# Performance work log

Hardware: AMD Instinct MI355X
Metric: run time of the kernel (lower is better)

## Reference

```python
import jax, jax.numpy as jnp
import numpy as np

H = 8            # num_heads
SIM_THRESH = 0.75


def setup_inputs() -> dict:
    key = jax.random.key(0)
    ks = jax.random.split(key, 6)
    B, N, C, CR = 1, 1536, 256, 64
    x_cls = jax.random.normal(ks[0], (B, N, C), dtype=jnp.float32)
    x_reg = jax.random.normal(ks[1], (B, N, CR), dtype=jnp.float32)
    cls_score = jax.random.uniform(ks[2], (N,), dtype=jnp.float32)
    fg_score = jax.random.uniform(ks[3], (1, 1, 1, N), dtype=jnp.float32)
    W_cls = jax.random.normal(ks[4], (C, 3 * C), dtype=jnp.float32) / np.sqrt(C).astype(np.float32)
    W_reg = jax.random.normal(ks[5], (CR, 3 * CR), dtype=jnp.float32) / np.sqrt(CR).astype(np.float32)
    return {"x_cls": x_cls, "x_reg": x_reg, "cls_score": cls_score,
            "fg_score": fg_score, "W_cls": W_cls, "W_reg": W_reg}


def _l2norm(t):
    return t / jnp.linalg.norm(t, axis=-1, keepdims=True)


def _split_qkv(x, W):
    B, N, C = x.shape
    qkv = (x @ W).reshape(B, N, 3, H, C // H).transpose(2, 0, 3, 1, 4)  # [3,B,H,N,hd]
    return qkv[0], qkv[1], qkv[2]


def reference(x_cls, x_reg, cls_score, fg_score, W_cls, W_reg):
    B, N, C = x_cls.shape
    CR = x_reg.shape[-1]
    scale = (C // H) ** -0.5  # note: torch code uses the cls head_dim scale for BOTH branches

    q, k, v = _split_qkv(x_cls, W_cls)
    qn, kn, vn = _l2norm(q), _l2norm(k), _l2norm(v)
    qr, kr, vr = _split_qkv(x_reg, W_reg)
    qrn, krn, vrn = _l2norm(qr), _l2norm(kr), _l2norm(vr)

    # cls_score broadcast: value cls_score[j] at position (i, j), as in torch's reshape+repeat
    cs = cls_score.reshape(1, 1, 1, N)
    cls_mask = (cs > jnp.swapaxes(cs, -2, -1) - 0.1).astype(jnp.float32)        # [1,1,N,N]
    fg_mask = (fg_score > jnp.swapaxes(fg_score, -2, -1) - 0.1).astype(jnp.float32)  # [1,1,N,N]

    # raw cosine-similarity matrices of the (normalized) value vectors
    attn_cls_raw = jnp.einsum('bhid,bhjd->bhij', vn, vn)   # [B,H,N,N]
    attn_reg_raw = jnp.einsum('bhid,bhjd->bhij', vrn, vrn)

    attn_cls = jax.nn.softmax(
        jnp.einsum('bhid,bhjd->bhij', qn, kn) * scale * cs * cls_mask, axis=-1)
    attn_reg = jax.nn.softmax(
        jnp.einsum('bhid,bhjd->bhij', qrn, krn) * scale, axis=-1)
    attn = (attn_cls + attn_reg) * 0.5

    # threshold masks (mask=True, use_mask=True, sim_thresh=0.75 defaults)
    sim_mask = (attn_cls_raw.mean(axis=1) > SIM_THRESH).astype(jnp.float32)    # [B,N,N]
    sim_mask = jnp.broadcast_to(sim_mask[:, None], (B, H, N, N))
    sim_mask = sim_mask * cls_mask[0, 0] * fg_mask[0, 0]
    obj_mask = (attn_reg_raw.mean(axis=1)[0] > SIM_THRESH).astype(jnp.float32)  # [N,N]

    attn = sim_mask * attn
    obj_mask = obj_mask * sim_mask                                   # [B,H,N,N]
    obj_mask = obj_mask / jnp.sum(obj_mask, axis=-1, keepdims=True)  # safe: diagonal always 1
    attn = obj_mask * attn

    x = jnp.einsum('bhij,bhjd->bhid', attn, v).transpose(0, 2, 1, 3).reshape(B, N, C)
    out_cls = jnp.concatenate([x, x_cls], axis=-1)                   # [B,N,2C]
    xr = jnp.einsum('bhij,bhjd->bhid', attn, vr).transpose(0, 2, 1, 3).reshape(B, N, CR)
    out_reg = jnp.concatenate([xr, x_reg], axis=-1)                  # [B,N,2*CR]
    return out_cls, out_reg, sim_mask, obj_mask
```

## Files before the change

kernel.cpp:

```cpp
#include <hip/hip_runtime.h>
#include <hip/hip_bf16.h>

#define NT 1536
#define SCALE 0.17677669529663687f

typedef __attribute__((ext_vector_type(8))) short bf16x8;
typedef __attribute__((ext_vector_type(4))) float f32x4;

static __device__ __forceinline__ unsigned short f2b(float x) {
    __hip_bfloat16 h = __float2bfloat16(x);
    union { __hip_bfloat16 b; unsigned short u; } cv; cv.b = h; return cv.u;
}
static __device__ __forceinline__ float b2f(unsigned short u) {
    union { float f; unsigned v; } c; c.v = ((unsigned)u) << 16; return c.f;
}

__global__ __launch_bounds__(256) void prep(
    const float* __restrict__ x_cls, const float* __restrict__ x_reg,
    const float* __restrict__ W_cls, const float* __restrict__ W_reg,
    unsigned short* __restrict__ xb_c, unsigned short* __restrict__ xb_r,
    unsigned short* __restrict__ Wt_c, unsigned short* __restrict__ Wt_r)
{
    const int u = blockIdx.x * 256 + threadIdx.x;
    if (u < 393216) {
        xb_c[u] = f2b(x_cls[u]);
    } else if (u < 491520) {
        const int v = u - 393216;
        xb_r[v] = f2b(x_reg[v]);
    } else if (u < 688128) {
        const int v = u - 491520;
        const int j = v >> 8, k = v & 255;
        Wt_c[v] = f2b(W_cls[k * 768 + j]);
    } else if (u < 700416) {
        const int v = u - 688128;
        const int j = v >> 6, k = v & 63;
        Wt_r[v] = f2b(W_reg[k * 192 + j]);
    }
}

__global__ __launch_bounds__(256) void gemm_mfma(
    const unsigned short* __restrict__ xb_c, const unsigned short* __restrict__ Wt_c,
    const unsigned short* __restrict__ xb_r, const unsigned short* __restrict__ Wt_r,
    float* __restrict__ qkv_c, unsigned short* __restrict__ qb_c,
    float* __restrict__ qkv_r, unsigned short* __restrict__ qb_r)
{
    const unsigned short *A, *B;
    float* qkv; unsigned short* qb;
    int K, NN, KS;
    const bool isreg = (blockIdx.z == 1);
    if (!isreg) { A = xb_c; B = Wt_c; qkv = qkv_c; qb = qb_c; K = 256; NN = 768; KS = 8; }
    else { if (blockIdx.x >= 3) return;
           A = xb_r; B = Wt_r; qkv = qkv_r; qb = qb_r; K = 64;  NN = 192; KS = 2; }
    __shared__ short Ai[64 * 40], Bj[64 * 40];
    const int t = threadIdx.x, lane = t & 63;
    const int wv = t >> 6, wr = wv >> 1, wc = wv & 1;
    const int i0 = blockIdx.y * 64, j0 = blockIdx.x * 64;
    const int srow = t >> 2, sc8 = (t & 3) * 8;
    f32x4 acc[2][2];
    #pragma unroll
    for (int a = 0; a < 2; a++)
        #pragma unroll
        for (int b = 0; b < 2; b++) acc[a][b] = (f32x4){0, 0, 0, 0};
    float4 ra = *(const float4*)&A[(i0 + srow) * K + sc8];
    float4 rb = *(const float4*)&B[(j0 + srow) * K + sc8];
    for (int ks = 0; ks < KS; ks++) {
        __syncthreads();
        *(float4*)&Ai[srow * 40 + sc8] = ra;
        *(float4*)&Bj[srow * 40 + sc8] = rb;
        if (ks + 1 < KS) {
            ra = *(const float4*)&A[(i0 + srow) * K + (ks + 1) * 32 + sc8];
            rb = *(const float4*)&B[(j0 + srow) * K + (ks + 1) * 32 + sc8];
        }
        __syncthreads();
        const int k8 = (lane >> 4) * 8;
        bf16x8 af[2], bf_[2];
        #pragma unroll
        for (int fr = 0; fr < 2; fr++)
            af[fr] = *(const bf16x8*)&Ai[(wr * 32 + fr * 16 + (lane & 15)) * 40 + k8];
        #pragma unroll
        for (int fc = 0; fc < 2; fc++)
            bf_[fc] = *(const bf16x8*)&Bj[(wc * 32 + fc * 16 + (lane & 15)) * 40 + k8];
        #pragma unroll
        for (int fr = 0; fr < 2; fr++)
            #pragma unroll
            for (int fc = 0; fc < 2; fc++)
                acc[fr][fc] = __builtin_amdgcn_mfma_f32_16x16x32_bf16(af[fr], bf_[fc], acc[fr][fc], 0, 0, 0);
    }
    #pragma unroll
    for (int fr = 0; fr < 2; fr++)
        #pragma unroll
        for (int r4 = 0; r4 < 4; r4++) {
            const int i = i0 + wr * 32 + fr * 16 + (lane >> 4) * 4 + r4;
            if (!isreg) {
                float s = acc[fr][0][r4] * acc[fr][0][r4] + acc[fr][1][r4] * acc[fr][1][r4];
                s += __shfl_xor(s, 1); s += __shfl_xor(s, 2);
                s += __shfl_xor(s, 4); s += __shfl_xor(s, 8);
                const float inv = 1.0f / sqrtf(s);
                #pragma unroll
                for (int fc = 0; fc < 2; fc++) {
                    const int j = j0 + wc * 32 + fc * 16 + (lane & 15);
                    const float v = acc[fr][fc][r4];
                    qkv[i * NN + j] = v;
                    qb[i * NN + j] = f2b(v * inv);
                }
            } else {
                #pragma unroll
                for (int fc = 0; fc < 2; fc++) {
                    const float v = acc[fr][fc][r4];
                    float s = v * v;
                    s += __shfl_xor(s, 1); s += __shfl_xor(s, 2); s += __shfl_xor(s, 4);
                    const float inv = 1.0f / sqrtf(s);
                    const int j = j0 + wc * 32 + fc * 16 + (lane & 15);
                    qkv[i * NN + j] = v;
                    qb[i * NN + j] = f2b(v * inv);
                }
            }
        }
}

__global__ __launch_bounds__(256) void bits_mfma(
    const unsigned short* __restrict__ qb_cls, const unsigned short* __restrict__ qb_reg,
    const float* __restrict__ cls_score, const float* __restrict__ fg_score,
    unsigned* __restrict__ simbits, unsigned* __restrict__ objbits)
{
    __shared__ short Ai[64 * 40], Bj[64 * 40];
    __shared__ float csi[64], csj[64], fgi[64], fgj[64];
    __shared__ unsigned simw[64][2], objw[64][2];
    const int t = threadIdx.x;
    const int lane = t & 63;
    const int wv = t >> 6, wr = wv >> 1, wc = wv & 1;
    const int i0 = blockIdx.y * 64, j0 = blockIdx.x * 64;
    if (t < 64)       { csi[t] = cls_score[i0 + t]; fgi[t] = fg_score[i0 + t]; }
    else if (t < 128) { csj[t - 64] = cls_score[j0 + t - 64]; fgj[t - 64] = fg_score[j0 + t - 64]; }
    const int sr = t >> 2, sc = t & 3;
    f32x4 ac[2][2], ar[2][2];
    #pragma unroll
    for (int a = 0; a < 2; a++)
        #pragma unroll
        for (int b = 0; b < 2; b++) { ac[a][b] = (f32x4){0,0,0,0}; ar[a][b] = (f32x4){0,0,0,0}; }
    float4 ra = *(const float4*)&qb_cls[(i0 + sr) * 768 + 512 + sc * 8];
    float4 rb = *(const float4*)&qb_cls[(j0 + sr) * 768 + 512 + sc * 8];
    for (int ks = 0; ks < 10; ks++) {
        __syncthreads();
        *(float4*)&Ai[sr * 40 + sc * 8] = ra;
        *(float4*)&Bj[sr * 40 + sc * 8] = rb;
        if (ks < 7) {
            ra = *(const float4*)&qb_cls[(i0 + sr) * 768 + 512 + (ks + 1) * 32 + sc * 8];
            rb = *(const float4*)&qb_cls[(j0 + sr) * 768 + 512 + (ks + 1) * 32 + sc * 8];
        } else if (ks < 9) {
            const int k2 = ks - 7;
            ra = *(const float4*)&qb_reg[(i0 + sr) * 192 + 128 + k2 * 32 + sc * 8];
            rb = *(const float4*)&qb_reg[(j0 + sr) * 192 + 128 + k2 * 32 + sc * 8];
        }
        __syncthreads();
        const int k8 = (lane >> 4) * 8;
        bf16x8 af[2], bf_[2];
        #pragma unroll
        for (int fr = 0; fr < 2; fr++)
            af[fr] = *(const bf16x8*)&Ai[(wr * 32 + fr * 16 + (lane & 15)) * 40 + k8];
        #pragma unroll
        for (int fc = 0; fc < 2; fc++)
            bf_[fc] = *(const bf16x8*)&Bj[(wc * 32 + fc * 16 + (lane & 15)) * 40 + k8];
        if (ks < 8) {
            #pragma unroll
            for (int fr = 0; fr < 2; fr++)
                #pragma unroll
                for (int fc = 0; fc < 2; fc++)
                    ac[fr][fc] = __builtin_amdgcn_mfma_f32_16x16x32_bf16(af[fr], bf_[fc], ac[fr][fc], 0, 0, 0);
        } else {
            #pragma unroll
            for (int fr = 0; fr < 2; fr++)
                #pragma unroll
                for (int fc = 0; fc < 2; fc++)
                    ar[fr][fc] = __builtin_amdgcn_mfma_f32_16x16x32_bf16(af[fr], bf_[fc], ar[fr][fc], 0, 0, 0);
        }
    }
    #pragma unroll
    for (int fr = 0; fr < 2; fr++)
        #pragma unroll
        for (int r4 = 0; r4 < 4; r4++) {
            const int rloc = wr * 32 + fr * 16 + (lane >> 4) * 4 + r4;
            const float ci = csi[rloc] - 0.1f, fgv = fgi[rloc] - 0.1f;
            unsigned sm[2], om[2];
            #pragma unroll
            for (int fc = 0; fc < 2; fc++) {
                const int cloc = wc * 32 + fc * 16 + (lane & 15);
                const bool clsb = csj[cloc] > ci;
                const bool fgb  = fgj[cloc] > fgv;
                const bool sim = (ac[fr][fc][r4] * 0.125f > 0.75f) && clsb && fgb;
                const bool obj = sim && (ar[fr][fc][r4] * 0.125f > 0.75f);
                unsigned long long bs = __ballot(sim);
                unsigned long long bo = __ballot(obj);
                const int g = lane >> 4;
                sm[fc] = (unsigned)((bs >> (16 * g)) & 0xFFFFull);
                om[fc] = (unsigned)((bo >> (16 * g)) & 0xFFFFull);
            }
            if ((lane & 15) == 0) {
                simw[rloc][wc] = sm[0] | (sm[1] << 16);
                objw[rloc][wc] = om[0] | (om[1] << 16);
            }
        }
    __syncthreads();
    if (t < 128) {
        const int row = t >> 1, w = t & 1;
        simbits[(i0 + row) * 48 + blockIdx.x * 2 + w] = simw[row][w];
        objbits[(i0 + row) * 48 + blockIdx.x * 2 + w] = objw[row][w];
    }
}

__global__ __launch_bounds__(256) void denom_expand(
    const unsigned short* __restrict__ qb_cls, const unsigned short* __restrict__ qb_reg,
    const float* __restrict__ cls_score,
    const unsigned* __restrict__ simbits, const unsigned* __restrict__ objbits,
    float* __restrict__ Dcpart, float* __restrict__ Drpart,
    float* __restrict__ sim_out, float* __restrict__ obj_out)
{
    __shared__ short Ai[64 * 40], Bj[64 * 40];
    __shared__ short Kr[64 * 72], Qr[64 * 72];
    __shared__ float csi[64], csj[64];
    __shared__ unsigned bw[6][48];
    __shared__ float invs[6];
    const int t = threadIdx.x;
    if (blockIdx.x < 576) {
        const int jB = blockIdx.x % 24, iB = blockIdx.x / 24;
        const int i0 = iB * 64, j0 = jB * 64;
        const int lane = t & 63;
        const int wv = t >> 6, wr = wv >> 1, wc = wv & 1;
        if (t < 64)       csj[t] = cls_score[j0 + t];
        else if (t < 128) csi[t - 64] = cls_score[i0 + t - 64];
        #pragma unroll
        for (int it = 0; it < 2; it++) {
            const int u = it * 256 + t;
            const int r = u >> 3, c = u & 7;
            *(float4*)&Kr[r * 72 + c * 8] = *(const float4*)&qb_reg[(j0 + r) * 192 + 64 + c * 8];
            *(float4*)&Qr[r * 72 + c * 8] = *(const float4*)&qb_reg[(i0 + r) * 192 + 0 + c * 8];
        }
        const int sr = t >> 2, sc = t & 3;
        __syncthreads();
        float cI[2], cJ[8];
        #pragma unroll
        for (int fc = 0; fc < 2; fc++) cI[fc] = csi[wc * 32 + fc * 16 + (lane & 15)] - 0.1f;
        #pragma unroll
        for (int fr = 0; fr < 2; fr++)
            #pragma unroll
            for (int r4 = 0; r4 < 4; r4++)
                cJ[fr * 4 + r4] = csj[wr * 32 + fr * 16 + (lane >> 4) * 4 + r4];
        float pC[2][8], pR[2][8];
        const bool g0 = (lane >> 4) == 0;
        const bf16x8 zz = {0, 0, 0, 0, 0, 0, 0, 0};
        float4 ra = *(const float4*)&qb_cls[(j0 + sr) * 768 + 256 + sc * 8];
        float4 rb = *(const float4*)&qb_cls[(i0 + sr) * 768 + 0   + sc * 8];
        for (int h = 0; h < 8; h++) {
            __syncthreads();
            *(float4*)&Ai[sr * 40 + sc * 8] = ra;
            *(float4*)&Bj[sr * 40 + sc * 8] = rb;
            if (h < 7) {
                ra = *(const float4*)&qb_cls[(j0 + sr) * 768 + 256 + (h + 1) * 32 + sc * 8];
                rb = *(const float4*)&qb_cls[(i0 + sr) * 768 + 0   + (h + 1) * 32 + sc * 8];
            }
            __syncthreads();
            const int k8 = (lane >> 4) * 8;
            bf16x8 a[2], b[2], arg[2], brg[2];
            #pragma unroll
            for (int fr = 0; fr < 2; fr++) {
                const int row = wr * 32 + fr * 16 + (lane & 15);
                a[fr] = *(const bf16x8*)&Ai[row * 40 + k8];
                arg[fr] = g0 ? *(const bf16x8*)&Kr[row * 72 + h * 8] : zz;
            }
            #pragma unroll
            for (int fc = 0; fc < 2; fc++) {
                const int row = wc * 32 + fc * 16 + (lane & 15);
                b[fc] = *(const bf16x8*)&Bj[row * 40 + k8];
                brg[fc] = g0 ? *(const bf16x8*)&Qr[row * 72 + h * 8] : zz;
            }
            f32x4 acc[2][2], racc[2][2];
            #pragma unroll
            for (int fr = 0; fr < 2; fr++)
                #pragma unroll
                for (int fc = 0; fc < 2; fc++) {
                    acc[fr][fc] = (f32x4){0,0,0,0};
                    racc[fr][fc] = (f32x4){0,0,0,0};
                    acc[fr][fc] = __builtin_amdgcn_mfma_f32_16x16x32_bf16(a[fr], b[fc], acc[fr][fc], 0, 0, 0);
                    racc[fr][fc] = __builtin_amdgcn_mfma_f32_16x16x32_bf16(arg[fr], brg[fc], racc[fr][fc], 0, 0, 0);
                }
            #pragma unroll
            for (int fc = 0; fc < 2; fc++) {
                float sC = 0.f, sR = 0.f;
                #pragma unroll
                for (int fr = 0; fr < 2; fr++)
                    #pragma unroll
                    for (int r4 = 0; r4 < 4; r4++) {
                        const float cj = cJ[fr * 4 + r4];
                        const float lc = (cj > cI[fc]) ? acc[fr][fc][r4] * SCALE * cj : 0.0f;
                        sC += __expf(lc);
                        sR += __expf(racc[fr][fc][r4] * SCALE);
                    }
                pC[fc][h] = sC; pR[fc][h] = sR;
            }
        }
        #pragma unroll
        for (int fc = 0; fc < 2; fc++)
            #pragma unroll
            for (int h = 0; h < 8; h++) {
                float v = pC[fc][h]; v += __shfl_xor(v, 16); v += __shfl_xor(v, 32);
                float u = pR[fc][h]; u += __shfl_xor(u, 16); u += __shfl_xor(u, 32);
                if (lane < 16) {
                    const int i = i0 + wc * 32 + fc * 16 + lane;
                    const int p = jB * 2 + wr;
                    Dcpart[(p * NT + i) * 8 + h] = v;
                    Drpart[(p * NT + i) * 8 + h] = u;
                }
            }
    } else {
        const int eb = blockIdx.x - 576;
        const int arr = eb >> 11;
        const int rem = eb & 2047;
        const int copy = rem >> 8;
        const int blk = rem & 255;
        const int r0 = blk * 6;
        const unsigned* src = arr ? objbits : simbits;
        for (int u = t; u < 288; u += 256) bw[u / 48][u % 48] = src[(r0 + u / 48) * 48 + (u % 48)];
        __syncthreads();
        if (t < 6) {
            int c = 0;
            #pragma unroll 8
            for (int w = 0; w < 48; w++) c += __popc(bw[t][w]);
            invs[t] = 1.0f / (float)c;
        }
        __syncthreads();
        f32x4* dst = (f32x4*)((arr ? obj_out : sim_out)
                              + (size_t)copy * NT * NT + (size_t)r0 * NT);
        #pragma unroll
        for (int rpt = 0; rpt < 9; rpt++) {
            const int u = rpt * 256 + t;
            const int row = u / 384;
            const int c4 = u - row * 384;
            const int j0 = c4 * 4;
            const unsigned w = bw[row][j0 >> 5] >> (j0 & 31);
            const float on = arr ? invs[row] : 1.0f;
            f32x4 v;
            v.x = (w & 1u) ? on : 0.f;
            v.y = (w & 2u) ? on : 0.f;
            v.z = (w & 4u) ? on : 0.f;
            v.w = (w & 8u) ? on : 0.f;
            __builtin_nontemporal_store(v, dst + u);
        }
    }
}

__global__ __launch_bounds__(256) void out_small(
    const float* __restrict__ qkv_cls, const unsigned short* __restrict__ qb_cls,
    const float* __restrict__ qkv_reg, const unsigned short* __restrict__ qb_reg,
    const float* __restrict__ cls_score,
    const unsigned* __restrict__ objbits,
    const float* __restrict__ Dcpart, const float* __restrict__ Drpart,
    const float* __restrict__ x_cls, const float* __restrict__ x_reg,
    float* __restrict__ out_cls, float* __restrict__ out_reg)
{
    const int i = (blockIdx.x << 2) + (threadIdx.x >> 6);
    const int l = threadIdx.x & 63;
    const int g = l >> 3;
    const ushort4 qu = *(const ushort4*)&qb_cls[i * 768 + 4 * l];
    const float qx = b2f(qu.x), qy = b2f(qu.y), qz = b2f(qu.z), qw = b2f(qu.w);
    const float qr = b2f(qb_reg[i * 192 + l]);
    unsigned myw = (l < 48) ? objbits[i * 48 + l] : 0u;
    int cnt = __popc(myw);
    #pragma unroll
    for (int m = 1; m < 64; m <<= 1) cnt += __shfl_xor(cnt, m);
    const int s = l & 7;
    float Dcv = 0.f, Drv = 0.f;
    #pragma unroll
    for (int p6 = 0; p6 < 6; p6++) {
        const int p = s * 6 + p6;
        Dcv += Dcpart[(p * NT + i) * 8 + g];
        Drv += Drpart[(p * NT + i) * 8 + g];
    }
    Dcv += __shfl_xor(Dcv, 1); Dcv += __shfl_xor(Dcv, 2); Dcv += __shfl_xor(Dcv, 4);
    Drv += __shfl_xor(Drv, 1); Drv += __shfl_xor(Drv, 2); Drv += __shfl_xor(Drv, 4);
    float a1x = 0.f, a1y = 0.f, a1z = 0.f, a1w = 0.f;
    float a2x = 0.f, a2y = 0.f, a2z = 0.f, a2w = 0.f;
    float rr1 = 0.f, rr2 = 0.f;
    for (int w = 0; w < 48; w++) {
        unsigned bits = __shfl(myw, w);
        while (bits) {
            const int b = __ffs(bits) - 1;
            bits &= bits - 1u;
            const int j = w * 32 + b;
            const ushort4 ku = *(const ushort4*)&qb_cls[j * 768 + 256 + 4 * l];
            const float4 v4 = *(const float4*)&qkv_cls[j * 768 + 512 + 4 * l];
            const float kr = b2f(qb_reg[j * 192 + 64 + l]);
            const float vr = qkv_reg[j * 192 + 128 + l];
            float dc = qx * b2f(ku.x) + qy * b2f(ku.y) + qz * b2f(ku.z) + qw * b2f(ku.w);
            dc += __shfl_xor(dc, 1); dc += __shfl_xor(dc, 2); dc += __shfl_xor(dc, 4);
            float dr = qr * kr;
            dr += __shfl_xor(dr, 1); dr += __shfl_xor(dr, 2); dr += __shfl_xor(dr, 4);
            const float cj = cls_score[j];
            const float ec = __expf(dc * SCALE * cj);
            const float er = __expf(dr * SCALE);
            a1x += ec * v4.x; a1y += ec * v4.y; a1z += ec * v4.z; a1w += ec * v4.w;
            a2x += er * v4.x; a2y += er * v4.y; a2z += er * v4.z; a2w += er * v4.w;
            rr1 += ec * vr;   rr2 += er * vr;
        }
    }
    const float iDc = 1.0f / Dcv, iDr = 1.0f / Drv;
    const float hi = 0.5f / (float)cnt;
    float4 o;
    o.x = (a1x * iDc + a2x * iDr) * hi;
    o.y = (a1y * iDc + a2y * iDr) * hi;
    o.z = (a1z * iDc + a2z * iDr) * hi;
    o.w = (a1w * iDc + a2w * iDr) * hi;
    *(float4*)&out_cls[i * 512 + 4 * l] = o;
    out_reg[i * 128 + l] = (rr1 * iDc + rr2 * iDr) * hi;
    *(float4*)&out_cls[i * 512 + 256 + 4 * l] = *(const float4*)&x_cls[i * 256 + 4 * l];
    out_reg[i * 128 + 64 + l] = x_reg[i * 64 + l];
}

extern "C" void kernel_launch(void* const* d_in, const int* in_sizes, int n_in,
                              void* d_out, int out_size, void* d_ws, size_t ws_size,
                              hipStream_t stream)
{
    (void)in_sizes; (void)n_in; (void)out_size; (void)ws_size;
    const float* x_cls     = (const float*)d_in[0];
    const float* x_reg     = (const float*)d_in[1];
    const float* cls_score = (const float*)d_in[2];
    const float* fg_score  = (const float*)d_in[3];
    const float* W_cls     = (const float*)d_in[4];
    const float* W_reg     = (const float*)d_in[5];

    float* out = (float*)d_out;
    float* out_cls = out;
    float* out_reg = out + 786432;
    float* sim_out = out + 983040;
    float* obj_out = out + 19857408;

    float* wsf = (float*)d_ws;
    float* qkv_cls = wsf;
    float* qkv_reg = wsf + 1179648;
    float* Dcpart  = wsf + 1474560;
    float* Drpart  = wsf + 2064384;
    unsigned short* qb_cls = (unsigned short*)(wsf + 2654208);
    unsigned short* qb_reg = (unsigned short*)(wsf + 3244032);
    unsigned short* xb_c   = (unsigned short*)(wsf + 3391488);
    unsigned short* xb_r   = (unsigned short*)(wsf + 3588096);
    unsigned short* Wt_c   = (unsigned short*)(wsf + 3637248);
    unsigned short* Wt_r   = (unsigned short*)(wsf + 3735552);
    unsigned* simbits = (unsigned*)(wsf + 3741696);
    unsigned* objbits = simbits + 73728;

    prep<<<2736, 256, 0, stream>>>(x_cls, x_reg, W_cls, W_reg, xb_c, xb_r, Wt_c, Wt_r);
    gemm_mfma<<<dim3(12, 24, 2), 256, 0, stream>>>(
        xb_c, Wt_c, xb_r, Wt_r, qkv_cls, qb_cls, qkv_reg, qb_reg);
    bits_mfma<<<dim3(24, 24), 256, 0, stream>>>(
        qb_cls, qb_reg, cls_score, fg_score, simbits, objbits);
    denom_expand<<<4672, 256, 0, stream>>>(
        qb_cls, qb_reg, cls_score, simbits, objbits,
        Dcpart, Drpart, sim_out, obj_out);
    out_small<<<384, 256, 0, stream>>>(
        qkv_cls, qb_cls, qkv_reg, qb_reg, cls_score,
        objbits, Dcpart, Drpart, x_cls, x_reg, out_cls, out_reg);
}
```

Measured before the change: 81.53 us.

## Regroup kernels into bits+denom and finish launches with two-stage register prefetch

Merges the bitmask MFMA kernel with the denominator computation into one launch, since neither depends on the other. The mask expansion moves out of the denominator kernel and shares a launch with the output accumulation. The launch count drops from five to four, and independent work can overlap within a grid. The GEMM and MFMA load loops also prefetch two K-slices ahead instead of one, at the cost of extra registers per thread.

```diff
diff --git a/kernel.cpp b/kernel.cpp
--- a/kernel.cpp
+++ b/kernel.cpp
@@ -61,15 +61,21 @@
     for (int a = 0; a < 2; a++)
         #pragma unroll
         for (int b = 0; b < 2; b++) acc[a][b] = (f32x4){0, 0, 0, 0};
-    float4 ra = *(const float4*)&A[(i0 + srow) * K + sc8];
-    float4 rb = *(const float4*)&B[(j0 + srow) * K + sc8];
+    float4 ra = *(const float4*)&A[(i0 + srow) * K + 0 * 32 + sc8];
+    float4 rb = *(const float4*)&B[(j0 + srow) * K + 0 * 32 + sc8];
+    float4 ra2, rb2;
+    if (KS > 1) {
+        ra2 = *(const float4*)&A[(i0 + srow) * K + 1 * 32 + sc8];
+        rb2 = *(const float4*)&B[(j0 + srow) * K + 1 * 32 + sc8];
+    }
     for (int ks = 0; ks < KS; ks++) {
         __syncthreads();
         *(float4*)&Ai[srow * 40 + sc8] = ra;
         *(float4*)&Bj[srow * 40 + sc8] = rb;
-        if (ks + 1 < KS) {
-            ra = *(const float4*)&A[(i0 + srow) * K + (ks + 1) * 32 + sc8];
-            rb = *(const float4*)&B[(j0 + srow) * K + (ks + 1) * 32 + sc8];
+        ra = ra2; rb = rb2;
+        if (ks + 2 < KS) {
+            ra2 = *(const float4*)&A[(i0 + srow) * K + (ks + 2) * 32 + sc8];
+            rb2 = *(const float4*)&B[(j0 + srow) * K + (ks + 2) * 32 + sc8];
         }
         __syncthreads();
         const int k8 = (lane >> 4) * 8;
@@ -118,114 +124,103 @@
         }
 }
 
-__global__ __launch_bounds__(256) void bits_mfma(
+__global__ __launch_bounds__(256) void bitsdenom(
     const unsigned short* __restrict__ qb_cls, const unsigned short* __restrict__ qb_reg,
     const float* __restrict__ cls_score, const float* __restrict__ fg_score,
-    unsigned* __restrict__ simbits, unsigned* __restrict__ objbits)
+    unsigned* __restrict__ simbits, unsigned* __restrict__ objbits,
+    float* __restrict__ Dcpart, float* __restrict__ Drpart)
 {
     __shared__ short Ai[64 * 40], Bj[64 * 40];
+    __shared__ short Kr[64 * 72], Qr[64 * 72];
     __shared__ float csi[64], csj[64], fgi[64], fgj[64];
     __shared__ unsigned simw[64][2], objw[64][2];
     const int t = threadIdx.x;
     const int lane = t & 63;
     const int wv = t >> 6, wr = wv >> 1, wc = wv & 1;
-    const int i0 = blockIdx.y * 64, j0 = blockIdx.x * 64;
-    if (t < 64)       { csi[t] = cls_score[i0 + t]; fgi[t] = fg_score[i0 + t]; }
-    else if (t < 128) { csj[t - 64] = cls_score[j0 + t - 64]; fgj[t - 64] = fg_score[j0 + t - 64]; }
     const int sr = t >> 2, sc = t & 3;
-    f32x4 ac[2][2], ar[2][2];
-    #pragma unroll
-    for (int a = 0; a < 2; a++)
-        #pragma unroll
-        for (int b = 0; b < 2; b++) { ac[a][b] = (f32x4){0,0,0,0}; ar[a][b] = (f32x4){0,0,0,0}; }
-    float4 ra = *(const float4*)&qb_cls[(i0 + sr) * 768 + 512 + sc * 8];
-    float4 rb = *(const float4*)&qb_cls[(j0 + sr) * 768 + 512 + sc * 8];
-    for (int ks = 0; ks < 10; ks++) {
-        __syncthreads();
-        *(float4*)&Ai[sr * 40 + sc * 8] = ra;
-        *(float4*)&Bj[sr * 40 + sc * 8] = rb;
-        if (ks < 7) {
-            ra = *(const float4*)&qb_cls[(i0 + sr) * 768 + 512 + (ks + 1) * 32 + sc * 8];
-            rb = *(const float4*)&qb_cls[(j0 + sr) * 768 + 512 + (ks + 1) * 32 + sc * 8];
-        } else if (ks < 9) {
-            const int k2 = ks - 7;
-            ra = *(const float4*)&qb_reg[(i0 + sr) * 192 + 128 + k2 * 32 + sc * 8];
-            rb = *(const float4*)&qb_reg[(j0 + sr) * 192 + 128 + k2 * 32 + sc * 8];
-        }
-        __syncthreads();
-        const int k8 = (lane >> 4) * 8;
-        bf16x8 af[2], bf_[2];
+
+    if (blockIdx.x < 576) {
+        const int iB = blockIdx.x / 24, jB = blockIdx.x % 24;
+        const int i0 = iB * 64, j0 = jB * 64;
+        if (t < 64)       { csi[t] = cls_score[i0 + t]; fgi[t] = fg_score[i0 + t]; }
+        else if (t < 128) { csj[t - 64] = cls_score[j0 + t - 64]; fgj[t - 64] = fg_score[j0 + t - 64]; }
+        f32x4 ac[2][2], ar[2][2];
+        #pragma unroll
+        for (int a = 0; a < 2; a++)
+            #pragma unroll
+            for (int b = 0; b < 2; b++) { ac[a][b] = (f32x4){0,0,0,0}; ar[a][b] = (f32x4){0,0,0,0}; }
+        #define LD_A(s) ((s) < 8 ? *(const float4*)&qb_cls[(i0 + sr) * 768 + 512 + (s) * 32 + sc * 8] \
+                                 : *(const float4*)&qb_reg[(i0 + sr) * 192 + 128 + ((s) - 8) * 32 + sc * 8])
+        #define LD_B(s) ((s) < 8 ? *(const float4*)&qb_cls[(j0 + sr) * 768 + 512 + (s) * 32 + sc * 8] \
+                                 : *(const float4*)&qb_reg[(j0 + sr) * 192 + 128 + ((s) - 8) * 32 + sc * 8])
+        float4 ra = LD_A(0), rb = LD_B(0);
+        float4 ra2 = LD_A(1), rb2 = LD_B(1);
+        for (int ks = 0; ks < 10; ks++) {
+            __syncthreads();
+            *(float4*)&Ai[sr * 40 + sc * 8] = ra;
+            *(float4*)&Bj[sr * 40 + sc * 8] = rb;
+            ra = ra2; rb = rb2;
+            if (ks + 2 < 10) { ra2 = LD_A(ks + 2); rb2 = LD_B(ks + 2); }
+            __syncthreads();
+            const int k8 = (lane >> 4) * 8;
+            bf16x8 af[2], bf_[2];
+            #pragma unroll
+            for (int fr = 0; fr < 2; fr++)
+                af[fr] = *(const bf16x8*)&Ai[(wr * 32 + fr * 16 + (lane & 15)) * 40 + k8];
+            #pragma unroll
+            for (int fc = 0; fc < 2; fc++)
+                bf_[fc] = *(const bf16x8*)&Bj[(wc * 32 + fc * 16 + (lane & 15)) * 40 + k8];
+            if (ks < 8) {
+                #pragma unroll
+                for (int fr = 0; fr < 2; fr++)
+                    #pragma unroll
+                    for (int fc = 0; fc < 2; fc++)
+                        ac[fr][fc] = __builtin_amdgcn_mfma_f32_16x16x32_bf16(af[fr], bf_[fc], ac[fr][fc], 0, 0, 0);
+            } else {
+                #pragma unroll
+                for (int fr = 0; fr < 2; fr++)
+                    #pragma unroll
+                    for (int fc = 0; fc < 2; fc++)
+                        ar[fr][fc] = __builtin_amdgcn_mfma_f32_16x16x32_bf16(af[fr], bf_[fc], ar[fr][fc], 0, 0, 0);
+            }
+        }
+        #undef LD_A
+        #undef LD_B
         #pragma unroll
         for (int fr = 0; fr < 2; fr++)
-            af[fr] = *(const bf16x8*)&Ai[(wr * 32 + fr * 16 + (lane & 15)) * 40 + k8];
-        #pragma unroll
-        for (int fc = 0; fc < 2; fc++)
-            bf_[fc] = *(const bf16x8*)&Bj[(wc * 32 + fc * 16 + (lane & 15)) * 40 + k8];
-        if (ks < 8) {
-            #pragma unroll
-            for (int fr = 0; fr < 2; fr++)
-                #pragma unroll
-                for (int fc = 0; fc < 2; fc++)
-                    ac[fr][fc] = __builtin_amdgcn_mfma_f32_16x16x32_bf16(af[fr], bf_[fc], ac[fr][fc], 0, 0, 0);
-        } else {
-            #pragma unroll
-            for (int fr = 0; fr < 2; fr++)
-                #pragma unroll
-                for (int fc = 0; fc < 2; fc++)
-                    ar[fr][fc] = __builtin_amdgcn_mfma_f32_16x16x32_bf16(af[fr], bf_[fc], ar[fr][fc], 0, 0, 0);
-        }
-    }
-    #pragma unroll
-    for (int fr = 0; fr < 2; fr++)
-        #pragma unroll
-        for (int r4 = 0; r4 < 4; r4++) {
-            const int rloc = wr * 32 + fr * 16 + (lane >> 4) * 4 + r4;
-            const float ci = csi[rloc] - 0.1f, fgv = fgi[rloc] - 0.1f;
-            unsigned sm[2], om[2];
-            #pragma unroll
-            for (int fc = 0; fc < 2; fc++) {
-                const int cloc = wc * 32 + fc * 16 + (lane & 15);
-                const bool clsb = csj[cloc] > ci;
-                const bool fgb  = fgj[cloc] > fgv;
-                const bool sim = (ac[fr][fc][r4] * 0.125f > 0.75f) && clsb && fgb;
-                const bool obj = sim && (ar[fr][fc][r4] * 0.125f > 0.75f);
-                unsigned long long bs = __ballot(sim);
-                unsigned long long bo = __ballot(obj);
-                const int g = lane >> 4;
-                sm[fc] = (unsigned)((bs >> (16 * g)) & 0xFFFFull);
-                om[fc] = (unsigned)((bo >> (16 * g)) & 0xFFFFull);
-            }
-            if ((lane & 15) == 0) {
-                simw[rloc][wc] = sm[0] | (sm[1] << 16);
-                objw[rloc][wc] = om[0] | (om[1] << 16);
-            }
-        }
-    __syncthreads();
-    if (t < 128) {
-        const int row = t >> 1, w = t & 1;
-        simbits[(i0 + row) * 48 + blockIdx.x * 2 + w] = simw[row][w];
-        objbits[(i0 + row) * 48 + blockIdx.x * 2 + w] = objw[row][w];
-    }
-}
-
-__global__ __launch_bounds__(256) void denom_expand(
-    const unsigned short* __restrict__ qb_cls, const unsigned short* __restrict__ qb_reg,
-    const float* __restrict__ cls_score,
-    const unsigned* __restrict__ simbits, const unsigned* __restrict__ objbits,
-    float* __restrict__ Dcpart, float* __restrict__ Drpart,
-    float* __restrict__ sim_out, float* __restrict__ obj_out)
-{
-    __shared__ short Ai[64 * 40], Bj[64 * 40];
-    __shared__ short Kr[64 * 72], Qr[64 * 72];
-    __shared__ float csi[64], csj[64];
-    __shared__ unsigned bw[6][48];
-    __shared__ float invs[6];
-    const int t = threadIdx.x;
-    if (blockIdx.x < 576) {
-        const int jB = blockIdx.x % 24, iB = blockIdx.x / 24;
+            #pragma unroll
+            for (int r4 = 0; r4 < 4; r4++) {
+                const int rloc = wr * 32 + fr * 16 + (lane >> 4) * 4 + r4;
+                const float ci = csi[rloc] - 0.1f, fgv = fgi[rloc] - 0.1f;
+                unsigned sm[2], om[2];
+                #pragma unroll
+                for (int fc = 0; fc < 2; fc++) {
+                    const int cloc = wc * 32 + fc * 16 + (lane & 15);
+                    const bool clsb = csj[cloc] > ci;
+                    const bool fgb  = fgj[cloc] > fgv;
+                    const bool sim = (ac[fr][fc][r4] * 0.125f > 0.75f) && clsb && fgb;
+                    const bool obj = sim && (ar[fr][fc][r4] * 0.125f > 0.75f);
+                    unsigned long long bs = __ballot(sim);
+                    unsigned long long bo = __ballot(obj);
+                    const int g = lane >> 4;
+                    sm[fc] = (unsigned)((bs >> (16 * g)) & 0xFFFFull);
+                    om[fc] = (unsigned)((bo >> (16 * g)) & 0xFFFFull);
+                }
+                if ((lane & 15) == 0) {
+                    simw[rloc][wc] = sm[0] | (sm[1] << 16);
+                    objw[rloc][wc] = om[0] | (om[1] << 16);
+                }
+            }
+        __syncthreads();
+        if (t < 128) {
+            const int row = t >> 1, w = t & 1;
+            simbits[(i0 + row) * 48 + jB * 2 + w] = simw[row][w];
+            objbits[(i0 + row) * 48 + jB * 2 + w] = objw[row][w];
+        }
+    } else {
+        const int vd = blockIdx.x - 576;
+        const int iB = vd / 24, jB = vd % 24;
         const int i0 = iB * 64, j0 = jB * 64;
-        const int lane = t & 63;
-        const int wv = t >> 6, wr = wv >> 1, wc = wv & 1;
         if (t < 64)       csj[t] = cls_score[j0 + t];
         else if (t < 128) csi[t - 64] = cls_score[i0 + t - 64];
         #pragma unroll
@@ -235,7 +230,6 @@
             *(float4*)&Kr[r * 72 + c * 8] = *(const float4*)&qb_reg[(j0 + r) * 192 + 64 + c * 8];
             *(float4*)&Qr[r * 72 + c * 8] = *(const float4*)&qb_reg[(i0 + r) * 192 + 0 + c * 8];
         }
-        const int sr = t >> 2, sc = t & 3;
         __syncthreads();
         float cI[2], cJ[8];
         #pragma unroll
@@ -248,15 +242,18 @@
         float pC[2][8], pR[2][8];
         const bool g0 = (lane >> 4) == 0;
         const bf16x8 zz = {0, 0, 0, 0, 0, 0, 0, 0};
-        float4 ra = *(const float4*)&qb_cls[(j0 + sr) * 768 + 256 + sc * 8];
-        float4 rb = *(const float4*)&qb_cls[(i0 + sr) * 768 + 0   + sc * 8];
+        float4 ra = *(const float4*)&qb_cls[(j0 + sr) * 768 + 256 + 0 * 32 + sc * 8];
+        float4 rb = *(const float4*)&qb_cls[(i0 + sr) * 768 + 0   + 0 * 32 + sc * 8];
+        float4 ra2 = *(const float4*)&qb_cls[(j0 + sr) * 768 + 256 + 1 * 32 + sc * 8];
+        float4 rb2 = *(const float4*)&qb_cls[(i0 + sr) * 768 + 0   + 1 * 32 + sc * 8];
         for (int h = 0; h < 8; h++) {
             __syncthreads();
             *(float4*)&Ai[sr * 40 + sc * 8] = ra;
             *(float4*)&Bj[sr * 40 + sc * 8] = rb;
-            if (h < 7) {
-                ra = *(const float4*)&qb_cls[(j0 + sr) * 768 + 256 + (h + 1) * 32 + sc * 8];
-                rb = *(const float4*)&qb_cls[(i0 + sr) * 768 + 0   + (h + 1) * 32 + sc * 8];
+            ra = ra2; rb = rb2;
+            if (h + 2 < 8) {
+                ra2 = *(const float4*)&qb_cls[(j0 + sr) * 768 + 256 + (h + 2) * 32 + sc * 8];
+                rb2 = *(const float4*)&qb_cls[(i0 + sr) * 768 + 0   + (h + 2) * 32 + sc * 8];
             }
             __syncthreads();
             const int k8 = (lane >> 4) * 8;
@@ -311,8 +308,81 @@
                     Drpart[(p * NT + i) * 8 + h] = u;
                 }
             }
+    }
+}
+
+__global__ __launch_bounds__(256) void finish(
+    const float* __restrict__ qkv_cls, const unsigned short* __restrict__ qb_cls,
+    const float* __restrict__ qkv_reg, const unsigned short* __restrict__ qb_reg,
+    const float* __restrict__ cls_score,
+    const unsigned* __restrict__ simbits, const unsigned* __restrict__ objbits,
+    const float* __restrict__ Dcpart, const float* __restrict__ Drpart,
+    const float* __restrict__ x_cls, const float* __restrict__ x_reg,
+    float* __restrict__ out_cls, float* __restrict__ out_reg,
+    float* __restrict__ sim_out, float* __restrict__ obj_out)
+{
+    __shared__ unsigned bw[6][48];
+    __shared__ float invs[6];
+    const int t = threadIdx.x;
+    if (blockIdx.x < 384) {
+        const int i = (blockIdx.x << 2) + (t >> 6);
+        const int l = t & 63;
+        const int g = l >> 3;
+        const ushort4 qu = *(const ushort4*)&qb_cls[i * 768 + 4 * l];
+        const float qx = b2f(qu.x), qy = b2f(qu.y), qz = b2f(qu.z), qw = b2f(qu.w);
+        const float qr = b2f(qb_reg[i * 192 + l]);
+        unsigned myw = (l < 48) ? objbits[i * 48 + l] : 0u;
+        int cnt = __popc(myw);
+        #pragma unroll
+        for (int m = 1; m < 64; m <<= 1) cnt += __shfl_xor(cnt, m);
+        const int s = l & 7;
+        float Dcv = 0.f, Drv = 0.f;
+        #pragma unroll
+        for (int p6 = 0; p6 < 6; p6++) {
+            const int p = s * 6 + p6;
+            Dcv += Dcpart[(p * NT + i) * 8 + g];
+            Drv += Drpart[(p * NT + i) * 8 + g];
+        }
+        Dcv += __shfl_xor(Dcv, 1); Dcv += __shfl_xor(Dcv, 2); Dcv += __shfl_xor(Dcv, 4);
+        Drv += __shfl_xor(Drv, 1); Drv += __shfl_xor(Drv, 2); Drv += __shfl_xor(Drv, 4);
+        float a1x = 0.f, a1y = 0.f, a1z = 0.f, a1w = 0.f;
+        float a2x = 0.f, a2y = 0.f, a2z = 0.f, a2w = 0.f;
+        float rr1 = 0.f, rr2 = 0.f;
+        for (int w = 0; w < 48; w++) {
+            unsigned bits = __shfl(myw, w);
+            while (bits) {
+                const int b = __ffs(bits) - 1;
+                bits &= bits - 1u;
+                const int j = w * 32 + b;
+                const ushort4 ku = *(const ushort4*)&qb_cls[j * 768 + 256 + 4 * l];
+                const float4 v4 = *(const float4*)&qkv_cls[j * 768 + 512 + 4 * l];
+                const float kr = b2f(qb_reg[j * 192 + 64 + l]);
+                const float vr = qkv_reg[j * 192 + 128 + l];
+                float dc = qx * b2f(ku.x) + qy * b2f(ku.y) + qz * b2f(ku.z) + qw * b2f(ku.w);
+                dc += __shfl_xor(dc, 1); dc += __shfl_xor(dc, 2); dc += __shfl_xor(dc, 4);
+                float dr = qr * kr;
+                dr += __shfl_xor(dr, 1); dr += __shfl_xor(dr, 2); dr += __shfl_xor(dr, 4);
+                const float cj = cls_score[j];
+                const float ec = __expf(dc * SCALE * cj);
+                const float er = __expf(dr * SCALE);
+                a1x += ec * v4.x; a1y += ec * v4.y; a1z += ec * v4.z; a1w += ec * v4.w;
+                a2x += er * v4.x; a2y += er * v4.y; a2z += er * v4.z; a2w += er * v4.w;
+                rr1 += ec * vr;   rr2 += er * vr;
+            }
+        }
+        const float iDc = 1.0f / Dcv, iDr = 1.0f / Drv;
+        const float hi = 0.5f / (float)cnt;
+        float4 o;
+        o.x = (a1x * iDc + a2x * iDr) * hi;
+        o.y = (a1y * iDc + a2y * iDr) * hi;
+        o.z = (a1z * iDc + a2z * iDr) * hi;
+        o.w = (a1w * iDc + a2w * iDr) * hi;
+        *(float4*)&out_cls[i * 512 + 4 * l] = o;
+        out_reg[i * 128 + l] = (rr1 * iDc + rr2 * iDr) * hi;
+        *(float4*)&out_cls[i * 512 + 256 + 4 * l] = *(const float4*)&x_cls[i * 256 + 4 * l];
+        out_reg[i * 128 + 64 + l] = x_reg[i * 64 + l];
     } else {
-        const int eb = blockIdx.x - 576;
+        const int eb = blockIdx.x - 384;
         const int arr = eb >> 11;
         const int rem = eb & 2047;
         const int copy = rem >> 8;
@@ -348,73 +418,6 @@
     }
 }
 
-__global__ __launch_bounds__(256) void out_small(
-    const float* __restrict__ qkv_cls, const unsigned short* __restrict__ qb_cls,
-    const float* __restrict__ qkv_reg, const unsigned short* __restrict__ qb_reg,
-    const float* __restrict__ cls_score,
-    const unsigned* __restrict__ objbits,
-    const float* __restrict__ Dcpart, const float* __restrict__ Drpart,
-    const float* __restrict__ x_cls, const float* __restrict__ x_reg,
-    float* __restrict__ out_cls, float* __restrict__ out_reg)
-{
-    const int i = (blockIdx.x << 2) + (threadIdx.x >> 6);
-    const int l = threadIdx.x & 63;
-    const int g = l >> 3;
-    const ushort4 qu = *(const ushort4*)&qb_cls[i * 768 + 4 * l];
-    const float qx = b2f(qu.x), qy = b2f(qu.y), qz = b2f(qu.z), qw = b2f(qu.w);
-    const float qr = b2f(qb_reg[i * 192 + l]);
-    unsigned myw = (l < 48) ? objbits[i * 48 + l] : 0u;
-    int cnt = __popc(myw);
-    #pragma unroll
-    for (int m = 1; m < 64; m <<= 1) cnt += __shfl_xor(cnt, m);
-    const int s = l & 7;
-    float Dcv = 0.f, Drv = 0.f;
-    #pragma unroll
-    for (int p6 = 0; p6 < 6; p6++) {
-        const int p = s * 6 + p6;
-        Dcv += Dcpart[(p * NT + i) * 8 + g];
-        Drv += Drpart[(p * NT + i) * 8 + g];
-    }
-    Dcv += __shfl_xor(Dcv, 1); Dcv += __shfl_xor(Dcv, 2); Dcv += __shfl_xor(Dcv, 4);
-    Drv += __shfl_xor(Drv, 1); Drv += __shfl_xor(Drv, 2); Drv += __shfl_xor(Drv, 4);
-    float a1x = 0.f, a1y = 0.f, a1z = 0.f, a1w = 0.f;
-    float a2x = 0.f, a2y = 0.f, a2z = 0.f, a2w = 0.f;
-    float rr1 = 0.f, rr2 = 0.f;
-    for (int w = 0; w < 48; w++) {
-        unsigned bits = __shfl(myw, w);
-        while (bits) {
-            const int b = __ffs(bits) - 1;
-            bits &= bits - 1u;
-            const int j = w * 32 + b;
-            const ushort4 ku = *(const ushort4*)&qb_cls[j * 768 + 256 + 4 * l];
-            const float4 v4 = *(const float4*)&qkv_cls[j * 768 + 512 + 4 * l];
-            const float kr = b2f(qb_reg[j * 192 + 64 + l]);
-            const float vr = qkv_reg[j * 192 + 128 + l];
-            float dc = qx * b2f(ku.x) + qy * b2f(ku.y) + qz * b2f(ku.z) + qw * b2f(ku.w);
-            dc += __shfl_xor(dc, 1); dc += __shfl_xor(dc, 2); dc += __shfl_xor(dc, 4);
-            float dr = qr * kr;
-            dr += __shfl_xor(dr, 1); dr += __shfl_xor(dr, 2); dr += __shfl_xor(dr, 4);
-            const float cj = cls_score[j];
-            const float ec = __expf(dc * SCALE * cj);
-            const float er = __expf(dr * SCALE);
-            a1x += ec * v4.x; a1y += ec * v4.y; a1z += ec * v4.z; a1w += ec * v4.w;
-            a2x += er * v4.x; a2y += er * v4.y; a2z += er * v4.z; a2w += er * v4.w;
-            rr1 += ec * vr;   rr2 += er * vr;
-        }
-    }
-    const float iDc = 1.0f / Dcv, iDr = 1.0f / Drv;
-    const float hi = 0.5f / (float)cnt;
-    float4 o;
-    o.x = (a1x * iDc + a2x * iDr) * hi;
-    o.y = (a1y * iDc + a2y * iDr) * hi;
-    o.z = (a1z * iDc + a2z * iDr) * hi;
-    o.w = (a1w * iDc + a2w * iDr) * hi;
-    *(float4*)&out_cls[i * 512 + 4 * l] = o;
-    out_reg[i * 128 + l] = (rr1 * iDc + rr2 * iDr) * hi;
-    *(float4*)&out_cls[i * 512 + 256 + 4 * l] = *(const float4*)&x_cls[i * 256 + 4 * l];
-    out_reg[i * 128 + 64 + l] = x_reg[i * 64 + l];
-}
-
 extern "C" void kernel_launch(void* const* d_in, const int* in_sizes, int n_in,
                               void* d_out, int out_size, void* d_ws, size_t ws_size,
                               hipStream_t stream)
@@ -450,12 +453,10 @@
     prep<<<2736, 256, 0, stream>>>(x_cls, x_reg, W_cls, W_reg, xb_c, xb_r, Wt_c, Wt_r);
     gemm_mfma<<<dim3(12, 24, 2), 256, 0, stream>>>(
         xb_c, Wt_c, xb_r, Wt_r, qkv_cls, qb_cls, qkv_reg, qb_reg);
-    bits_mfma<<<dim3(24, 24), 256, 0, stream>>>(
-        qb_cls, qb_reg, cls_score, fg_score, simbits, objbits);
-    denom_expand<<<4672, 256, 0, stream>>>(
-        qb_cls, qb_reg, cls_score, simbits, objbits,
-        Dcpart, Drpart, sim_out, obj_out);
-    out_small<<<384, 256, 0, stream>>>(
+    bitsdenom<<<1152, 256, 0, stream>>>(
+        qb_cls, qb_reg, cls_score, fg_score, simbits, objbits, Dcpart, Drpart);
+    finish<<<4480, 256, 0, stream>>>(
         qkv_cls, qb_cls, qkv_reg, qb_reg, cls_score,
-        objbits, Dcpart, Drpart, x_cls, x_reg, out_cls, out_reg);
-}
+        simbits, objbits, Dcpart, Drpart, x_cls, x_reg,
+        out_cls, out_reg, sim_out, obj_out);
+}
```

Result: no change. 81.84 us (+0.4%).
